# Kernel optimization log

Measured on AMD Instinct MI355X. Metric: run time of the kernel, lower is better.

## Reference

```python
import jax, jax.numpy as jnp
import numpy as np


def setup_inputs() -> dict:
    key = jax.random.key(0)
    k1, k2 = jax.random.split(key)
    img = jax.random.normal(k1, (4, 96, 256, 256), dtype=jnp.float32)
    light = jax.random.normal(k2, (4, 96, 256, 256), dtype=jnp.float32)
    return {"img": img, "light": light}


def reference(img, light):
    B, C, H, W = img.shape
    F = C // 3
    # NCHW -> NHWC -> [B,H,W,F,3]
    im = img.transpose(0, 2, 3, 1).reshape(B, H, W, F, 3)
    lt = light.transpose(0, 2, 3, 1).reshape(B, H, W, F, 3)
    # per-light intensity magnitude: [B,H,W,F,1]
    I = jnp.linalg.norm(im, axis=-1, keepdims=True)
    # L^T I : [B,H,W,3,1]
    LtI = jnp.einsum('bhwfc,bhwfo->bhwco', lt, I)
    # L^T L : [B,H,W,3,3]
    LtL = jnp.einsum('bhwfc,bhwfd->bhwcd', lt, lt)
    Linv = jnp.linalg.inv(LtL)
    # normal estimate: [B,H,W,3]
    N = jnp.einsum('bhwcd,bhwdo->bhwco', Linv, LtI)[..., 0]
    N = N / (jnp.linalg.norm(N, axis=-1, keepdims=True) + 1e-10)
    # NHWC -> NCHW
    return N.transpose(0, 3, 1, 2)
```

## Files before the change

kernel.cpp:

```cpp
#include <hip/hip_runtime.h>


constexpr int QROW = 16384;
constexpr int CH   = 96;

__device__ __forceinline__ float fc(const float4 v, int j) {
    return j == 0 ? v.x : j == 1 ? v.y : j == 2 ? v.z : v.w;
}
__device__ __forceinline__ void setc(float4& v, int j, float x) {
    if (j == 0) v.x = x; else if (j == 1) v.y = x; else if (j == 2) v.z = x; else v.w = x;
}

__global__ __launch_bounds__(256, 4) void LS_44160853737780_kernel(
    const float4* __restrict__ img,
    const float4* __restrict__ light,
    float4* __restrict__ out)
{
    int t   = blockIdx.x * blockDim.x + threadIdx.x;
    int q   = t >> 2;
    int sub = t & 3;
    int b   = q >> 14;
    int p   = q & 16383;

    const float4* ib = img   + (size_t)(b * CH + sub * 24) * QROW + p;
    const float4* lb = light + (size_t)(b * CH + sub * 24) * QROW + p;

    float A00[4] = {0,0,0,0}, A01[4] = {0,0,0,0}, A02[4] = {0,0,0,0},
          A11[4] = {0,0,0,0}, A12[4] = {0,0,0,0}, A22[4] = {0,0,0,0},
          r0[4]  = {0,0,0,0}, r1[4]  = {0,0,0,0}, r2[4]  = {0,0,0,0};

    #pragma unroll
    for (int f = 0; f < 8; f += 2) {
        float4 i0x = ib[(3*f+0)*QROW], i0y = ib[(3*f+1)*QROW], i0z = ib[(3*f+2)*QROW];
        float4 i1x = ib[(3*f+3)*QROW], i1y = ib[(3*f+4)*QROW], i1z = ib[(3*f+5)*QROW];
        float4 l0x = lb[(3*f+0)*QROW], l0y = lb[(3*f+1)*QROW], l0z = lb[(3*f+2)*QROW];
        float4 l1x = lb[(3*f+3)*QROW], l1y = lb[(3*f+4)*QROW], l1z = lb[(3*f+5)*QROW];
        #pragma unroll
        for (int j = 0; j < 4; ++j) {
            {
                float x = fc(i0x,j), y = fc(i0y,j), z = fc(i0z,j);
                float I = sqrtf(x*x + y*y + z*z);
                float a = fc(l0x,j), c = fc(l0y,j), d = fc(l0z,j);
                A00[j] += a*a; A01[j] += a*c; A02[j] += a*d;
                A11[j] += c*c; A12[j] += c*d; A22[j] += d*d;
                r0[j]  += a*I; r1[j]  += c*I; r2[j]  += d*I;
            }
            {
                float x = fc(i1x,j), y = fc(i1y,j), z = fc(i1z,j);
                float I = sqrtf(x*x + y*y + z*z);
                float a = fc(l1x,j), c = fc(l1y,j), d = fc(l1z,j);
                A00[j] += a*a; A01[j] += a*c; A02[j] += a*d;
                A11[j] += c*c; A12[j] += c*d; A22[j] += d*d;
                r0[j]  += a*I; r1[j]  += c*I; r2[j]  += d*I;
            }
        }
    }

    #pragma unroll
    for (int m = 1; m <= 2; m <<= 1) {
        #pragma unroll
        for (int j = 0; j < 4; ++j) {
            A00[j] += __shfl_xor(A00[j], m);
            A01[j] += __shfl_xor(A01[j], m);
            A02[j] += __shfl_xor(A02[j], m);
            A11[j] += __shfl_xor(A11[j], m);
            A12[j] += __shfl_xor(A12[j], m);
            A22[j] += __shfl_xor(A22[j], m);
            r0[j]  += __shfl_xor(r0[j],  m);
            r1[j]  += __shfl_xor(r1[j],  m);
            r2[j]  += __shfl_xor(r2[j],  m);
        }
    }

    float4 o0, o1, o2;
    #pragma unroll
    for (int j = 0; j < 4; ++j) {
        float a00 = A00[j], a01 = A01[j], a02 = A02[j],
              a11 = A11[j], a12 = A12[j], a22 = A22[j];
        float c00 = a11*a22 - a12*a12;
        float c01 = a02*a12 - a01*a22;
        float c02 = a01*a12 - a02*a11;
        float c11 = a00*a22 - a02*a02;
        float c12 = a01*a02 - a00*a12;
        float c22 = a00*a11 - a01*a01;
        float det = a00*c00 + a01*c01 + a02*c02;
        float inv = 1.0f / det;
        float n0 = (c00*r0[j] + c01*r1[j] + c02*r2[j]) * inv;
        float n1 = (c01*r0[j] + c11*r1[j] + c12*r2[j]) * inv;
        float n2 = (c02*r0[j] + c12*r1[j] + c22*r2[j]) * inv;
        float nn = sqrtf(n0*n0 + n1*n1 + n2*n2);
        float s  = 1.0f / (nn + 1e-10f);
        setc(o0, j, n0*s);
        setc(o1, j, n1*s);
        setc(o2, j, n2*s);
    }

    if (sub < 3) {
        float4 v = (sub == 0) ? o0 : (sub == 1) ? o1 : o2;
        out[(size_t)(b * 3 + sub) * QROW + p] = v;
    }
}

extern "C" void kernel_launch(void* const* d_in, const int* in_sizes, int n_in,
                              void* d_out, int out_size, void* d_ws, size_t ws_size,
                              hipStream_t stream) {
    const float4* img   = (const float4*)d_in[0];
    const float4* light = (const float4*)d_in[1];
    float4* out = (float4*)d_out;
    LS_44160853737780_kernel<<<dim3(1024), dim3(256), 0, stream>>>(img, light, out);
}
```

Before: 213.6 us.

## Split channel groups across wavefronts with LDS reduction and XCD-aware block swizzle

Each 256-thread block now handles 64 consecutive pixel quads, with each of its four wavefronts covering one quarter of the channels. Before, each group of four adjacent lanes split the channels, so a single wave load touched four channel rows at once. The new layout makes every wave load one contiguous 1KB row segment, and partial sums are combined through shared memory instead of cross-lane shuffles. Blocks are also swizzled so that consecutive blocks on the same XCD map to contiguous pixel ranges. The cost is a __syncthreads plus LDS traffic, and three of the four waves sit idle during the solve and store phase. The loop now loads 6 float4s per iteration instead of 12, which may reduce memory-level parallelism.

```diff
diff --git a/kernel.cpp b/kernel.cpp
--- a/kernel.cpp
+++ b/kernel.cpp
@@ -2,7 +2,6 @@
 
 
 constexpr int QROW = 16384;
-constexpr int CH   = 96;
 
 __device__ __forceinline__ float fc(const float4 v, int j) {
     return j == 0 ? v.x : j == 1 ? v.y : j == 2 ? v.z : v.w;
@@ -16,59 +15,62 @@
     const float4* __restrict__ light,
     float4* __restrict__ out)
 {
-    int t   = blockIdx.x * blockDim.x + threadIdx.x;
-    int q   = t >> 2;
-    int sub = t & 3;
-    int b   = q >> 14;
-    int p   = q & 16383;
+    __shared__ float red[3][64][37];
 
-    const float4* ib = img   + (size_t)(b * CH + sub * 24) * QROW + p;
-    const float4* lb = light + (size_t)(b * CH + sub * 24) * QROW + p;
+    int blk  = blockIdx.x;
+    int swz  = (blk & 7) * 128 + (blk >> 3);
+    int b    = swz >> 8;
+    int p0   = (swz & 255) * 64;
+    int lane = threadIdx.x & 63;
+    int w    = threadIdx.x >> 6;
+    int p    = p0 + lane;
+
+    const float4* ib = img   + (size_t)(b * 96 + w * 24) * QROW + p;
+    const float4* lb = light + (size_t)(b * 96 + w * 24) * QROW + p;
 
     float A00[4] = {0,0,0,0}, A01[4] = {0,0,0,0}, A02[4] = {0,0,0,0},
           A11[4] = {0,0,0,0}, A12[4] = {0,0,0,0}, A22[4] = {0,0,0,0},
           r0[4]  = {0,0,0,0}, r1[4]  = {0,0,0,0}, r2[4]  = {0,0,0,0};
 
     #pragma unroll
-    for (int f = 0; f < 8; f += 2) {
-        float4 i0x = ib[(3*f+0)*QROW], i0y = ib[(3*f+1)*QROW], i0z = ib[(3*f+2)*QROW];
-        float4 i1x = ib[(3*f+3)*QROW], i1y = ib[(3*f+4)*QROW], i1z = ib[(3*f+5)*QROW];
-        float4 l0x = lb[(3*f+0)*QROW], l0y = lb[(3*f+1)*QROW], l0z = lb[(3*f+2)*QROW];
-        float4 l1x = lb[(3*f+3)*QROW], l1y = lb[(3*f+4)*QROW], l1z = lb[(3*f+5)*QROW];
+    for (int f = 0; f < 8; ++f) {
+        float4 ix = ib[(3*f+0)*QROW];
+        float4 iy = ib[(3*f+1)*QROW];
+        float4 iz = ib[(3*f+2)*QROW];
+        float4 lx = lb[(3*f+0)*QROW];
+        float4 ly = lb[(3*f+1)*QROW];
+        float4 lz = lb[(3*f+2)*QROW];
         #pragma unroll
         for (int j = 0; j < 4; ++j) {
-            {
-                float x = fc(i0x,j), y = fc(i0y,j), z = fc(i0z,j);
-                float I = sqrtf(x*x + y*y + z*z);
-                float a = fc(l0x,j), c = fc(l0y,j), d = fc(l0z,j);
-                A00[j] += a*a; A01[j] += a*c; A02[j] += a*d;
-                A11[j] += c*c; A12[j] += c*d; A22[j] += d*d;
-                r0[j]  += a*I; r1[j]  += c*I; r2[j]  += d*I;
-            }
-            {
-                float x = fc(i1x,j), y = fc(i1y,j), z = fc(i1z,j);
-                float I = sqrtf(x*x + y*y + z*z);
-                float a = fc(l1x,j), c = fc(l1y,j), d = fc(l1z,j);
-                A00[j] += a*a; A01[j] += a*c; A02[j] += a*d;
-                A11[j] += c*c; A12[j] += c*d; A22[j] += d*d;
-                r0[j]  += a*I; r1[j]  += c*I; r2[j]  += d*I;
-            }
+            float x = fc(ix,j), y = fc(iy,j), z = fc(iz,j);
+            float I = sqrtf(x*x + y*y + z*z);
+            float a = fc(lx,j), c = fc(ly,j), d = fc(lz,j);
+            A00[j] += a*a; A01[j] += a*c; A02[j] += a*d;
+            A11[j] += c*c; A12[j] += c*d; A22[j] += d*d;
+            r0[j]  += a*I; r1[j]  += c*I; r2[j]  += d*I;
         }
     }
 
-    #pragma unroll
-    for (int m = 1; m <= 2; m <<= 1) {
+    if (w > 0) {
+        float* dst = red[w - 1][lane];
         #pragma unroll
         for (int j = 0; j < 4; ++j) {
-            A00[j] += __shfl_xor(A00[j], m);
-            A01[j] += __shfl_xor(A01[j], m);
-            A02[j] += __shfl_xor(A02[j], m);
-            A11[j] += __shfl_xor(A11[j], m);
-            A12[j] += __shfl_xor(A12[j], m);
-            A22[j] += __shfl_xor(A22[j], m);
-            r0[j]  += __shfl_xor(r0[j],  m);
-            r1[j]  += __shfl_xor(r1[j],  m);
-            r2[j]  += __shfl_xor(r2[j],  m);
+            dst[0*4+j] = A00[j]; dst[1*4+j] = A01[j]; dst[2*4+j] = A02[j];
+            dst[3*4+j] = A11[j]; dst[4*4+j] = A12[j]; dst[5*4+j] = A22[j];
+            dst[6*4+j] = r0[j];  dst[7*4+j] = r1[j];  dst[8*4+j] = r2[j];
+        }
+    }
+    __syncthreads();
+    if (w != 0) return;
+
+    #pragma unroll
+    for (int s = 0; s < 3; ++s) {
+        const float* src = red[s][lane];
+        #pragma unroll
+        for (int j = 0; j < 4; ++j) {
+            A00[j] += src[0*4+j]; A01[j] += src[1*4+j]; A02[j] += src[2*4+j];
+            A11[j] += src[3*4+j]; A12[j] += src[4*4+j]; A22[j] += src[5*4+j];
+            r0[j]  += src[6*4+j]; r1[j]  += src[7*4+j]; r2[j]  += src[8*4+j];
         }
     }
 
@@ -95,15 +97,16 @@
         setc(o2, j, n2*s);
     }
 
-    if (sub < 3) {
-        float4 v = (sub == 0) ? o0 : (sub == 1) ? o1 : o2;
-        out[(size_t)(b * 3 + sub) * QROW + p] = v;
-    }
+    float4* ob = out + (size_t)(b * 3) * QROW + p;
+    ob[0]        = o0;
+    ob[QROW]     = o1;
+    ob[2 * QROW] = o2;
 }
 
 extern "C" void kernel_launch(void* const* d_in, const int* in_sizes, int n_in,
                               void* d_out, int out_size, void* d_ws, size_t ws_size,
                               hipStream_t stream) {
+    (void)in_sizes; (void)n_in; (void)out_size; (void)d_ws; (void)ws_size;
     const float4* img   = (const float4*)d_in[0];
     const float4* light = (const float4*)d_in[1];
     float4* out = (float4*)d_out;
```

Result: no change. 216.3 us (+1.2%).
